# Kernel tuning notes

Measured on AMD Instinct MI355X. Metric: run time of the kernel, lower is better.

Reference implementation:

```python
import jax, jax.numpy as jnp
import numpy as np

SLOPE = 25.0   # fast_sigmoid surrogate slope
THR = 1.0      # snntorch Leaky default threshold


@jax.custom_vjp
def spike(x):
    # Heaviside forward, fast-sigmoid surrogate backward
    return (x > 0).astype(x.dtype)

def _spike_fwd(x):
    return spike(x), x

def _spike_bwd(x, g):
    return (g / (SLOPE * jnp.abs(x) + 1.0) ** 2,)

spike.defvjp(_spike_fwd, _spike_bwd)


def conv2d(x, w, b):
    y = jax.lax.conv_general_dilated(
        x, w, window_strides=(1, 1), padding=((1, 1), (1, 1)),
        dimension_numbers=('NCHW', 'OIHW', 'NCHW'))
    return y + b[None, :, None, None]


def maxpool2(x):
    return jax.lax.reduce_window(x, -jnp.inf, jax.lax.max,
                                 (1, 1, 2, 2), (1, 1, 2, 2), 'VALID')


def bn_inf(x, g, b, m, v):
    # inference-mode BatchNorm2d, eps = 1e-5
    inv = g * jax.lax.rsqrt(v + 1e-5)
    return x * inv[None, :, None, None] + (b - m * inv)[None, :, None, None]


def lif_step(mem, inp, beta):
    # snntorch Leaky, reset_mechanism='subtract', learn_beta (clamped to [0,1])
    b = jnp.clip(beta, 0.0, 1.0)
    reset = jax.lax.stop_gradient((mem > THR).astype(mem.dtype))
    mem_new = b * mem + inp - reset * THR
    spk = spike(mem_new - THR)
    return spk, mem_new


def setup_inputs() -> dict:
    key = jax.random.key(0)
    ks = jax.random.split(key, 20)
    T, B, H, W = 25, 512, 100, 64   # T steps, batch, MAX_LEN, N_MELS
    NUM_CLASSES = 35
    FLAT = 32 * (H // 4) * (W // 4)  # 12800
    f32 = jnp.float32
    inp = {
        'x': jax.random.normal(ks[0], (T, B, H, W), f32),
        'conv1_w': jax.random.normal(ks[1], (16, 1, 3, 3), f32) * 0.2,
        'conv1_b': jnp.zeros((16,), f32),
        'bn1_g': jnp.ones((16,), f32),
        'bn1_b': jnp.zeros((16,), f32),
        'bn1_m': jax.random.normal(ks[2], (16,), f32) * 0.1,
        'bn1_v': jax.random.uniform(ks[3], (16,), f32) + 0.5,
        'conv2_w': jax.random.normal(ks[4], (32, 16, 3, 3), f32) * (1.0 / np.sqrt(16 * 9)),
        'conv2_b': jnp.zeros((32,), f32),
        'bn2_g': jnp.ones((32,), f32),
        'bn2_b': jnp.zeros((32,), f32),
        'bn2_m': jax.random.normal(ks[5], (32,), f32) * 0.1,
        'bn2_v': jax.random.uniform(ks[6], (32,), f32) + 0.5,
        'fc1_w': jax.random.normal(ks[7], (256, FLAT), f32) * (1.0 / np.sqrt(FLAT)),
        'fc1_b': jnp.zeros((256,), f32),
        'fc2_w': jax.random.normal(ks[8], (128, 256), f32) * (1.0 / np.sqrt(256)),
        'fc2_b': jnp.zeros((128,), f32),
        'fc3_w': jax.random.normal(ks[9], (NUM_CLASSES, 128), f32) * (1.0 / np.sqrt(128)),
        'fc3_b': jnp.zeros((NUM_CLASSES,), f32),
        'beta1': jnp.float32(0.9),
        'beta2': jnp.float32(0.9),
        'beta3': jnp.float32(0.9),
    }
    return inp


def reference(x, conv1_w, conv1_b, bn1_g, bn1_b, bn1_m, bn1_v,
              conv2_w, conv2_b, bn2_g, bn2_b, bn2_m, bn2_v,
              fc1_w, fc1_b, fc2_w, fc2_b, fc3_w, fc3_b,
              beta1, beta2, beta3):
    T, B = x.shape[0], x.shape[1]
    # CNN runs once on the time-averaged input
    x_mean = jnp.mean(x, axis=0)[:, None]          # (B, 1, H, W)
    f = maxpool2(jax.nn.relu(bn_inf(conv2d(x_mean, conv1_w, conv1_b), bn1_g, bn1_b, bn1_m, bn1_v)))
    f = maxpool2(jax.nn.relu(bn_inf(conv2d(f, conv2_w, conv2_b), bn2_g, bn2_b, bn2_m, bn2_v)))
    feat = f.reshape(B, -1)                        # (B, FLAT)
    # fc1 input is the same every step (dropout = identity in eval)
    cur1 = feat @ fc1_w.T + fc1_b                  # (B, 256)

    m1 = jnp.zeros((B, fc1_w.shape[0]), x.dtype)
    m2 = jnp.zeros((B, fc2_w.shape[0]), x.dtype)
    m3 = jnp.zeros((B, fc3_w.shape[0]), x.dtype)

    def step(carry, _):
        m1, m2, m3 = carry
        spk1, m1 = lif_step(m1, cur1, beta1)
        spk2, m2 = lif_step(m2, spk1 @ fc2_w.T + fc2_b, beta2)
        spk3, m3 = lif_step(m3, spk2 @ fc3_w.T + fc3_b, beta3)
        return (m1, m2, m3), spk3

    _, out = jax.lax.scan(step, (m1, m2, m3), None, length=T)
    return out                                     # (T, B, NUM_CLASSES)
```

## Files before the change

kernel.cpp:

```cpp
#include <hip/hip_runtime.h>

#define N_P1    (512*16*50*32)
#define N_FEAT  (512*12800)
#define N_PART  (32*512*256)

#define WS_P1    0
#define WS_FEAT  (WS_P1 + N_P1)
#define WS_PART  (WS_FEAT + N_FEAT)
#define WS_S1    0
#define WS_IN2   3276800
#define WS_S2    4915200

__global__ __launch_bounds__(256) void conv1_kernel(const float* __restrict__ x,
                                                    const float* __restrict__ w1,
                                                    const float* __restrict__ cb1,
                                                    const float* __restrict__ g1,
                                                    const float* __restrict__ bb1,
                                                    const float* __restrict__ m1g,
                                                    const float* __restrict__ v1,
                                                    float* __restrict__ p1) {
    __shared__ float xs[22 * 66];
    __shared__ float w1s[144];
    __shared__ float sh1s[16];
    const int b = blockIdx.x, s = blockIdx.y;
    const int tid = threadIdx.x;
    if (tid < 144) {
        int c = tid / 9;
        float inv = g1[c] * rsqrtf(v1[c] + 1e-5f);
        w1s[tid] = w1[tid] * inv;
    }
    if (tid < 16) {
        float inv = g1[tid] * rsqrtf(v1[tid] + 1e-5f);
        sh1s[tid] = cb1[tid] * inv + bb1[tid] - m1g[tid] * inv;
    }
    if (tid < 44) xs[(tid >> 1) * 66 + (tid & 1) * 65] = 0.f;
    const int r0 = s * 20 - 1;
    const size_t TSTR = (size_t)512 * 6400;
    for (int i = tid; i < 22 * 16; i += 256) {
        int lr = i >> 4, cq = i & 15;
        int gr = r0 + lr;
        float4 a0 = make_float4(0.f, 0.f, 0.f, 0.f), a1 = a0, a2 = a0, a3 = a0;
        if (gr >= 0 && gr < 100) {
            const float* px = x + (size_t)b * 6400 + gr * 64 + cq * 4;
            #pragma unroll
            for (int tt = 0; tt < 24; tt += 4) {
                float4 v0 = *(const float4*)(px + (size_t)(tt + 0) * TSTR);
                float4 v1_ = *(const float4*)(px + (size_t)(tt + 1) * TSTR);
                float4 v2_ = *(const float4*)(px + (size_t)(tt + 2) * TSTR);
                float4 v3 = *(const float4*)(px + (size_t)(tt + 3) * TSTR);
                a0.x += v0.x; a0.y += v0.y; a0.z += v0.z; a0.w += v0.w;
                a1.x += v1_.x; a1.y += v1_.y; a1.z += v1_.z; a1.w += v1_.w;
                a2.x += v2_.x; a2.y += v2_.y; a2.z += v2_.z; a2.w += v2_.w;
                a3.x += v3.x; a3.y += v3.y; a3.z += v3.z; a3.w += v3.w;
            }
            float4 v = *(const float4*)(px + (size_t)24 * TSTR);
            a0.x += v.x; a0.y += v.y; a0.z += v.z; a0.w += v.w;
        }
        const float sc = 1.0f / 25.0f;
        float* d = &xs[lr * 66 + 1 + cq * 4];
        d[0] = (a0.x + a1.x + a2.x + a3.x) * sc;
        d[1] = (a0.y + a1.y + a2.y + a3.y) * sc;
        d[2] = (a0.z + a1.z + a2.z + a3.z) * sc;
        d[3] = (a0.w + a1.w + a2.w + a3.w) * sc;
    }
    __syncthreads();
    for (int pos = tid; pos < 320; pos += 256) {
        int phl = pos >> 5, pw = pos & 31;
        int ph = s * 10 + phl;
        float win[4][4];
        #pragma unroll
        for (int a = 0; a < 4; ++a)
            #pragma unroll
            for (int c2 = 0; c2 < 4; ++c2)
                win[a][c2] = xs[(2 * phl + a) * 66 + 2 * pw + c2];
        #pragma unroll 1
        for (int c = 0; c < 16; ++c) {
            float s00 = 0.f, s01 = 0.f, s10 = 0.f, s11 = 0.f;
            #pragma unroll
            for (int dh = 0; dh < 3; ++dh)
                #pragma unroll
                for (int dw = 0; dw < 3; ++dw) {
                    float w = w1s[c * 9 + dh * 3 + dw];
                    s00 = fmaf(win[dh][dw],         w, s00);
                    s01 = fmaf(win[dh][dw + 1],     w, s01);
                    s10 = fmaf(win[dh + 1][dw],     w, s10);
                    s11 = fmaf(win[dh + 1][dw + 1], w, s11);
                }
            float m = fmaxf(fmaxf(s00, s01), fmaxf(s10, s11));
            float val = fmaxf(m + sh1s[c], 0.f);
            p1[(((size_t)b * 16 + c) * 50 + ph) * 32 + pw] = val;
        }
    }
}

__global__ __launch_bounds__(320) void conv2_kernel(const float* __restrict__ p1,
                                                    const float* __restrict__ w2g,
                                                    const float* __restrict__ cb2,
                                                    const float* __restrict__ g2,
                                                    const float* __restrict__ bb2,
                                                    const float* __restrict__ m2g,
                                                    const float* __restrict__ v2,
                                                    float* __restrict__ feat) {
    __shared__ float ins[16 * 12 * 36];
    __shared__ float wl[16 * 9 * 32];
    __shared__ float sh2s[32];
    const int b = blockIdx.x, s = blockIdx.y;
    const int tid = threadIdx.x;
    const int chg = tid & 15, q = (tid >> 4) & 3, phl = tid >> 6;
    const int ph = s * 5 + phl;

    for (int i = tid; i < 192; i += 320) {
        int ci = i / 12, lr = i - ci * 12;
        int gr = s * 10 - 1 + lr;
        float* dst = &ins[(ci * 12 + lr) * 36];
        if (gr >= 0 && gr < 50) {
            const float* src = p1 + (((size_t)b * 16 + ci) * 50 + gr) * 32;
            float4 v0 = *(const float4*)src;
            dst[0] = 0.f; dst[1] = v0.x; dst[2] = v0.y; dst[3] = v0.z;
            #pragma unroll
            for (int qq = 1; qq < 8; ++qq) {
                float4 v = *(const float4*)(src + 4 * qq - 1);
                *(float4*)(dst + 4 * qq) = v;
            }
            dst[32] = src[31];
            dst[33] = 0.f; dst[34] = 0.f; dst[35] = 0.f;
        } else {
            #pragma unroll
            for (int qq = 0; qq < 9; ++qq) *(float4*)(dst + 4 * qq) = make_float4(0.f, 0.f, 0.f, 0.f);
        }
    }
    for (int i = tid; i < 4608; i += 320) {
        int c = i / 144, rem = i - c * 144;
        float inv = g2[c] * rsqrtf(v2[c] + 1e-5f);
        wl[rem * 32 + c] = w2g[i] * inv;
    }
    if (tid < 32) {
        float inv = g2[tid] * rsqrtf(v2[tid] + 1e-5f);
        sh2s[tid] = cb2[tid] * inv + bb2[tid] - m2g[tid] * inv;
    }
    __syncthreads();

    float acc[2][2][8];
    #pragma unroll
    for (int c = 0; c < 2; ++c)
        #pragma unroll
        for (int a = 0; a < 2; ++a)
            #pragma unroll
            for (int xx = 0; xx < 8; ++xx) acc[c][a][xx] = 0.f;
    const int xb = q * 8;
    #pragma unroll 1
    for (int ci = 0; ci < 16; ++ci) {
        float2 wv[9];
        #pragma unroll
        for (int t = 0; t < 9; ++t)
            wv[t] = *(const float2*)&wl[(ci * 9 + t) * 32 + 2 * chg];
        #pragma unroll
        for (int lr4 = 0; lr4 < 4; ++lr4) {
            const float* row = &ins[(ci * 12 + (2 * phl + lr4)) * 36 + xb];
            float v[10];
            float4 t0 = *(const float4*)&row[0];
            float4 t1 = *(const float4*)&row[4];
            float2 t2 = *(const float2*)&row[8];
            v[0]=t0.x; v[1]=t0.y; v[2]=t0.z; v[3]=t0.w;
            v[4]=t1.x; v[5]=t1.y; v[6]=t1.z; v[7]=t1.w;
            v[8]=t2.x; v[9]=t2.y;
            #pragma unroll
            for (int a = 0; a < 2; ++a) {
                const int dh = lr4 - a;
                if (dh >= 0 && dh <= 2) {
                    #pragma unroll
                    for (int dw = 0; dw < 3; ++dw) {
                        float w0 = wv[dh * 3 + dw].x;
                        float w1 = wv[dh * 3 + dw].y;
                        #pragma unroll
                        for (int xx = 0; xx < 8; ++xx) {
                            acc[0][a][xx] = fmaf(v[xx + dw], w0, acc[0][a][xx]);
                            acc[1][a][xx] = fmaf(v[xx + dw], w1, acc[1][a][xx]);
                        }
                    }
                }
            }
        }
    }
    #pragma unroll
    for (int ch = 0; ch < 2; ++ch) {
        const int c = 2 * chg + ch;
        const float sh = sh2s[c];
        #pragma unroll
        for (int p = 0; p < 4; ++p) {
            float m = fmaxf(fmaxf(acc[ch][0][2 * p], acc[ch][0][2 * p + 1]),
                            fmaxf(acc[ch][1][2 * p], acc[ch][1][2 * p + 1]));
            float val = fmaxf(m + sh, 0.f);
            feat[(((size_t)b * 32 + c) * 25 + ph) * 16 + q * 4 + p] = val;
        }
    }
}

__global__ __launch_bounds__(256) void fc1_kernel(const float* __restrict__ feat,
                                                  const float* __restrict__ w,
                                                  float* __restrict__ part) {
    __shared__ float As[16 * 68];
    __shared__ float Bs[16 * 136];
    const int bx = blockIdx.x, by = blockIdx.y, bz = blockIdx.z;
    const int tid = threadIdx.x;
    const int tm = tid >> 4, tn = tid & 15;
    const int r = tid >> 2, cq = tid & 3;
    const int m0 = bx * 64, n0 = by * 128;
    const size_t aBase = (size_t)(m0 + r) * 12800 + bz * 400 + cq * 4;
    const size_t bBase = (size_t)(n0 + r) * 12800 + bz * 400 + cq * 4;
    float acc[4][8];
    #pragma unroll
    for (int i = 0; i < 4; ++i)
        #pragma unroll
        for (int j = 0; j < 8; ++j) acc[i][j] = 0.f;

    for (int kt = 0; kt < 25; ++kt) {
        float4 a0 = *(const float4*)(feat + aBase + kt * 16);
        float4 b0 = *(const float4*)(w    + bBase + kt * 16);
        float4 b1 = *(const float4*)(w    + bBase + (size_t)64 * 12800 + kt * 16);
        __syncthreads();
        As[(cq * 4 + 0) * 68 + r] = a0.x; As[(cq * 4 + 1) * 68 + r] = a0.y;
        As[(cq * 4 + 2) * 68 + r] = a0.z; As[(cq * 4 + 3) * 68 + r] = a0.w;
        Bs[(cq * 4 + 0) * 136 + r]      = b0.x; Bs[(cq * 4 + 1) * 136 + r]      = b0.y;
        Bs[(cq * 4 + 2) * 136 + r]      = b0.z; Bs[(cq * 4 + 3) * 136 + r]      = b0.w;
        Bs[(cq * 4 + 0) * 136 + 64 + r] = b1.x; Bs[(cq * 4 + 1) * 136 + 64 + r] = b1.y;
        Bs[(cq * 4 + 2) * 136 + 64 + r] = b1.z; Bs[(cq * 4 + 3) * 136 + 64 + r] = b1.w;
        __syncthreads();
        #pragma unroll
        for (int kk = 0; kk < 16; ++kk) {
            float4 av  = *(const float4*)&As[kk * 68 + tm * 4];
            float4 bv0 = *(const float4*)&Bs[kk * 136 + tn * 8];
            float4 bv1 = *(const float4*)&Bs[kk * 136 + tn * 8 + 4];
            float a_[4] = {av.x, av.y, av.z, av.w};
            float b_[8] = {bv0.x, bv0.y, bv0.z, bv0.w, bv1.x, bv1.y, bv1.z, bv1.w};
            #pragma unroll
            for (int i = 0; i < 4; ++i)
                #pragma unroll
                for (int j = 0; j < 8; ++j)
                    acc[i][j] = fmaf(a_[i], b_[j], acc[i][j]);
        }
    }
    #pragma unroll
    for (int i = 0; i < 4; ++i) {
        float* dst = &part[(size_t)bz * 131072 + (size_t)(m0 + tm * 4 + i) * 256 + n0 + tn * 8];
        *(float4*)dst       = make_float4(acc[i][0], acc[i][1], acc[i][2], acc[i][3]);
        *(float4*)(dst + 4) = make_float4(acc[i][4], acc[i][5], acc[i][6], acc[i][7]);
    }
}

__global__ __launch_bounds__(256) void lif1_kernel(const float* __restrict__ part,
                                                   const float* __restrict__ b1g,
                                                   const float* __restrict__ pb1,
                                                   float* __restrict__ S1) {
    const int i = blockIdx.x * 256 + threadIdx.x;
    const int k = i & 255;
    float cu = b1g[k];
    #pragma unroll 8
    for (int z = 0; z < 32; ++z) cu += part[(size_t)z * 131072 + i];
    const float be = fminf(fmaxf(pb1[0], 0.f), 1.f);
    float m = 0.f;
    #pragma unroll
    for (int t = 0; t < 25; ++t) {
        float r = (m > 1.f) ? 1.f : 0.f;
        m = fmaf(be, m, cu) - r;
        S1[(size_t)t * 131072 + i] = (m > 1.f) ? 1.f : 0.f;
    }
}

__global__ __launch_bounds__(256) void fc2g_kernel(const float* __restrict__ S1,
                                                   const float* __restrict__ w2g,
                                                   const float* __restrict__ b2g,
                                                   float* __restrict__ in2) {
    __shared__ float As[16 * 36];
    __shared__ float Bs[16 * 136];
    const int m0 = blockIdx.x * 32;
    const int tid = threadIdx.x;
    const int tm = tid >> 4, tn = tid & 15;
    float acc[2][8];
    #pragma unroll
    for (int i = 0; i < 2; ++i)
        #pragma unroll
        for (int j = 0; j < 8; ++j) acc[i][j] = 0.f;

    for (int kt = 0; kt < 16; ++kt) {
        float4 av = make_float4(0.f, 0.f, 0.f, 0.f);
        if (tid < 128) {
            int r = tid >> 2, cq = tid & 3;
            av = *(const float4*)&S1[(size_t)(m0 + r) * 256 + kt * 16 + cq * 4];
        }
        int rb = tid >> 1, kb = (tid & 1) * 8;
        float4 bv0 = *(const float4*)&w2g[rb * 256 + kt * 16 + kb];
        float4 bv1 = *(const float4*)&w2g[rb * 256 + kt * 16 + kb + 4];
        __syncthreads();
        if (tid < 128) {
            int r = tid >> 2, cq = tid & 3;
            As[(cq * 4 + 0) * 36 + r] = av.x; As[(cq * 4 + 1) * 36 + r] = av.y;
            As[(cq * 4 + 2) * 36 + r] = av.z; As[(cq * 4 + 3) * 36 + r] = av.w;
        }
        Bs[(kb + 0) * 136 + rb] = bv0.x; Bs[(kb + 1) * 136 + rb] = bv0.y;
        Bs[(kb + 2) * 136 + rb] = bv0.z; Bs[(kb + 3) * 136 + rb] = bv0.w;
        Bs[(kb + 4) * 136 + rb] = bv1.x; Bs[(kb + 5) * 136 + rb] = bv1.y;
        Bs[(kb + 6) * 136 + rb] = bv1.z; Bs[(kb + 7) * 136 + rb] = bv1.w;
        __syncthreads();
        #pragma unroll
        for (int kk = 0; kk < 16; ++kk) {
            float2 a2 = *(const float2*)&As[kk * 36 + tm * 2];
            float4 bv0_ = *(const float4*)&Bs[kk * 136 + tn * 8];
            float4 bv1_ = *(const float4*)&Bs[kk * 136 + tn * 8 + 4];
            float b_[8] = {bv0_.x, bv0_.y, bv0_.z, bv0_.w, bv1_.x, bv1_.y, bv1_.z, bv1_.w};
            #pragma unroll
            for (int j = 0; j < 8; ++j) {
                acc[0][j] = fmaf(a2.x, b_[j], acc[0][j]);
                acc[1][j] = fmaf(a2.y, b_[j], acc[1][j]);
            }
        }
    }
    float4 bb0 = *(const float4*)&b2g[tn * 8];
    float4 bb1 = *(const float4*)&b2g[tn * 8 + 4];
    #pragma unroll
    for (int i = 0; i < 2; ++i) {
        float* dst = &in2[(size_t)(m0 + tm * 2 + i) * 128 + tn * 8];
        *(float4*)dst       = make_float4(acc[i][0] + bb0.x, acc[i][1] + bb0.y,
                                          acc[i][2] + bb0.z, acc[i][3] + bb0.w);
        *(float4*)(dst + 4) = make_float4(acc[i][4] + bb1.x, acc[i][5] + bb1.y,
                                          acc[i][6] + bb1.z, acc[i][7] + bb1.w);
    }
}

__global__ __launch_bounds__(256) void lif2_kernel(const float* __restrict__ in2,
                                                   const float* __restrict__ pb2,
                                                   float* __restrict__ S2) {
    const int i = blockIdx.x * 256 + threadIdx.x;
    const float be = fminf(fmaxf(pb2[0], 0.f), 1.f);
    float m = 0.f;
    #pragma unroll
    for (int t = 0; t < 25; ++t) {
        float r = (m > 1.f) ? 1.f : 0.f;
        m = fmaf(be, m, in2[(size_t)t * 65536 + i]) - r;
        S2[(size_t)t * 65536 + i] = (m > 1.f) ? 1.f : 0.f;
    }
}

__global__ __launch_bounds__(64) void fc3l_kernel(const float* __restrict__ S2,
                                                  const float* __restrict__ w3g,
                                                  const float* __restrict__ b3g,
                                                  const float* __restrict__ pb3,
                                                  float* __restrict__ out) {
    __shared__ float w3T[128 * 36];
    __shared__ float s2row[128];
    const int b = blockIdx.x;
    const int lane = threadIdx.x;
    for (int i = lane; i < 4480; i += 64) {
        int j = i >> 7, k = i & 127;
        w3T[k * 36 + j] = w3g[i];
    }
    const float be = fminf(fmaxf(pb3[0], 0.f), 1.f);
    const float bias = (lane < 35) ? b3g[lane] : 0.f;
    float m = 0.f;
    __syncthreads();
    for (int t = 0; t < 25; ++t) {
        float2 v = *(const float2*)&S2[(size_t)t * 65536 + b * 128 + lane * 2];
        *(float2*)&s2row[lane * 2] = v;
        __syncthreads();
        if (lane < 35) {
            float a = bias;
            #pragma unroll 8
            for (int k = 0; k < 128; ++k)
                a = fmaf(s2row[k], w3T[k * 36 + lane], a);
            float r = (m > 1.f) ? 1.f : 0.f;
            m = fmaf(be, m, a) - r;
            out[((size_t)t * 512 + b) * 35 + lane] = (m > 1.f) ? 1.f : 0.f;
        }
        __syncthreads();
    }
}

extern "C" void kernel_launch(void* const* d_in, const int* in_sizes, int n_in,
                              void* d_out, int out_size, void* d_ws, size_t ws_size,
                              hipStream_t stream) {
    const float* x     = (const float*)d_in[0];
    const float* c1w   = (const float*)d_in[1];
    const float* c1b   = (const float*)d_in[2];
    const float* bn1g  = (const float*)d_in[3];
    const float* bn1b  = (const float*)d_in[4];
    const float* bn1m  = (const float*)d_in[5];
    const float* bn1v  = (const float*)d_in[6];
    const float* c2w   = (const float*)d_in[7];
    const float* c2b   = (const float*)d_in[8];
    const float* bn2g  = (const float*)d_in[9];
    const float* bn2b  = (const float*)d_in[10];
    const float* bn2m  = (const float*)d_in[11];
    const float* bn2v  = (const float*)d_in[12];
    const float* fc1w  = (const float*)d_in[13];
    const float* fc1b  = (const float*)d_in[14];
    const float* fc2w  = (const float*)d_in[15];
    const float* fc2b  = (const float*)d_in[16];
    const float* fc3w  = (const float*)d_in[17];
    const float* fc3b  = (const float*)d_in[18];
    const float* beta1 = (const float*)d_in[19];
    const float* beta2 = (const float*)d_in[20];
    const float* beta3 = (const float*)d_in[21];
    float* ws  = (float*)d_ws;
    float* out = (float*)d_out;

    conv1_kernel<<<dim3(512, 5), 256, 0, stream>>>(x, c1w, c1b, bn1g, bn1b, bn1m, bn1v,
                                                   ws + WS_P1);
    conv2_kernel<<<dim3(512, 5), 320, 0, stream>>>(ws + WS_P1, c2w, c2b, bn2g, bn2b, bn2m, bn2v,
                                                   ws + WS_FEAT);
    fc1_kernel<<<dim3(8, 2, 32), 256, 0, stream>>>(ws + WS_FEAT, fc1w, ws + WS_PART);
    lif1_kernel<<<512, 256, 0, stream>>>(ws + WS_PART, fc1b, beta1, ws + WS_S1);
    fc2g_kernel<<<400, 256, 0, stream>>>(ws + WS_S1, fc2w, fc2b, ws + WS_IN2);
    lif2_kernel<<<256, 256, 0, stream>>>(ws + WS_IN2, beta2, ws + WS_S2);
    fc3l_kernel<<<512, 64, 0, stream>>>(ws + WS_S2, fc3w, fc3b, beta3, out);
}
```

Before: 328.0 us.

## Enlarge fc1 tiles, prefetch GEMM loads, split fc3 into GEMM plus LIF kernels

conv1 now runs with 384 threads so each thread handles one input load slot and one output position instead of looping. fc1 moves to a 128x128 tile with an 8x8 per-thread micro-tile and register prefetch of the next K slice. fc2 gets the same register-prefetch double buffering. The serial per-batch fc3+LIF kernel is replaced by a batched GEMM over all 25 time steps followed by an elementwise LIF scan. This aims to raise arithmetic intensity and parallelism, at the cost of higher register pressure in fc1 and an extra workspace round trip for fc3.

```diff
diff --git a/kernel.cpp b/kernel.cpp
--- a/kernel.cpp
+++ b/kernel.cpp
@@ -10,8 +10,9 @@
 #define WS_S1    0
 #define WS_IN2   3276800
 #define WS_S2    4915200
-
-__global__ __launch_bounds__(256) void conv1_kernel(const float* __restrict__ x,
+#define WS_IN3   6553600
+
+__global__ __launch_bounds__(384) void conv1_kernel(const float* __restrict__ x,
                                                     const float* __restrict__ w1,
                                                     const float* __restrict__ cb1,
                                                     const float* __restrict__ g1,
@@ -29,15 +30,19 @@
         float inv = g1[c] * rsqrtf(v1[c] + 1e-5f);
         w1s[tid] = w1[tid] * inv;
     }
-    if (tid < 16) {
-        float inv = g1[tid] * rsqrtf(v1[tid] + 1e-5f);
-        sh1s[tid] = cb1[tid] * inv + bb1[tid] - m1g[tid] * inv;
-    }
-    if (tid < 44) xs[(tid >> 1) * 66 + (tid & 1) * 65] = 0.f;
+    if (tid >= 144 && tid < 160) {
+        int c = tid - 144;
+        float inv = g1[c] * rsqrtf(v1[c] + 1e-5f);
+        sh1s[c] = cb1[c] * inv + bb1[c] - m1g[c] * inv;
+    }
+    if (tid >= 160 && tid < 204) {
+        int q = tid - 160;
+        xs[(q >> 1) * 66 + (q & 1) * 65] = 0.f;
+    }
     const int r0 = s * 20 - 1;
     const size_t TSTR = (size_t)512 * 6400;
-    for (int i = tid; i < 22 * 16; i += 256) {
-        int lr = i >> 4, cq = i & 15;
+    if (tid < 352) {
+        int lr = tid >> 4, cq = tid & 15;
         int gr = r0 + lr;
         float4 a0 = make_float4(0.f, 0.f, 0.f, 0.f), a1 = a0, a2 = a0, a3 = a0;
         if (gr >= 0 && gr < 100) {
@@ -64,8 +69,8 @@
         d[3] = (a0.w + a1.w + a2.w + a3.w) * sc;
     }
     __syncthreads();
-    for (int pos = tid; pos < 320; pos += 256) {
-        int phl = pos >> 5, pw = pos & 31;
+    if (tid < 320) {
+        int phl = tid >> 5, pw = tid & 31;
         int ph = s * 10 + phl;
         float win[4][4];
         #pragma unroll
@@ -199,50 +204,57 @@
 __global__ __launch_bounds__(256) void fc1_kernel(const float* __restrict__ feat,
                                                   const float* __restrict__ w,
                                                   float* __restrict__ part) {
-    __shared__ float As[16 * 68];
+    __shared__ float As[16 * 136];
     __shared__ float Bs[16 * 136];
     const int bx = blockIdx.x, by = blockIdx.y, bz = blockIdx.z;
     const int tid = threadIdx.x;
     const int tm = tid >> 4, tn = tid & 15;
     const int r = tid >> 2, cq = tid & 3;
-    const int m0 = bx * 64, n0 = by * 128;
+    const int m0 = bx * 128, n0 = by * 128;
     const size_t aBase = (size_t)(m0 + r) * 12800 + bz * 400 + cq * 4;
     const size_t bBase = (size_t)(n0 + r) * 12800 + bz * 400 + cq * 4;
-    float acc[4][8];
-    #pragma unroll
-    for (int i = 0; i < 4; ++i)
-        #pragma unroll
-        for (int j = 0; j < 8; ++j) acc[i][j] = 0.f;
+    float acc[8][8] = {};
+    float4 a0 = *(const float4*)(feat + aBase);
+    float4 a1 = *(const float4*)(feat + aBase + (size_t)64 * 12800);
+    float4 b0 = *(const float4*)(w    + bBase);
+    float4 b1 = *(const float4*)(w    + bBase + (size_t)64 * 12800);
 
     for (int kt = 0; kt < 25; ++kt) {
-        float4 a0 = *(const float4*)(feat + aBase + kt * 16);
-        float4 b0 = *(const float4*)(w    + bBase + kt * 16);
-        float4 b1 = *(const float4*)(w    + bBase + (size_t)64 * 12800 + kt * 16);
-        __syncthreads();
-        As[(cq * 4 + 0) * 68 + r] = a0.x; As[(cq * 4 + 1) * 68 + r] = a0.y;
-        As[(cq * 4 + 2) * 68 + r] = a0.z; As[(cq * 4 + 3) * 68 + r] = a0.w;
+        __syncthreads();
+        As[(cq * 4 + 0) * 136 + r]      = a0.x; As[(cq * 4 + 1) * 136 + r]      = a0.y;
+        As[(cq * 4 + 2) * 136 + r]      = a0.z; As[(cq * 4 + 3) * 136 + r]      = a0.w;
+        As[(cq * 4 + 0) * 136 + 64 + r] = a1.x; As[(cq * 4 + 1) * 136 + 64 + r] = a1.y;
+        As[(cq * 4 + 2) * 136 + 64 + r] = a1.z; As[(cq * 4 + 3) * 136 + 64 + r] = a1.w;
         Bs[(cq * 4 + 0) * 136 + r]      = b0.x; Bs[(cq * 4 + 1) * 136 + r]      = b0.y;
         Bs[(cq * 4 + 2) * 136 + r]      = b0.z; Bs[(cq * 4 + 3) * 136 + r]      = b0.w;
         Bs[(cq * 4 + 0) * 136 + 64 + r] = b1.x; Bs[(cq * 4 + 1) * 136 + 64 + r] = b1.y;
         Bs[(cq * 4 + 2) * 136 + 64 + r] = b1.z; Bs[(cq * 4 + 3) * 136 + 64 + r] = b1.w;
         __syncthreads();
+        if (kt < 24) {
+            const int o = (kt + 1) * 16;
+            a0 = *(const float4*)(feat + aBase + o);
+            a1 = *(const float4*)(feat + aBase + (size_t)64 * 12800 + o);
+            b0 = *(const float4*)(w    + bBase + o);
+            b1 = *(const float4*)(w    + bBase + (size_t)64 * 12800 + o);
+        }
         #pragma unroll
         for (int kk = 0; kk < 16; ++kk) {
-            float4 av  = *(const float4*)&As[kk * 68 + tm * 4];
+            float4 av0 = *(const float4*)&As[kk * 136 + tm * 8];
+            float4 av1 = *(const float4*)&As[kk * 136 + tm * 8 + 4];
             float4 bv0 = *(const float4*)&Bs[kk * 136 + tn * 8];
             float4 bv1 = *(const float4*)&Bs[kk * 136 + tn * 8 + 4];
-            float a_[4] = {av.x, av.y, av.z, av.w};
+            float a_[8] = {av0.x, av0.y, av0.z, av0.w, av1.x, av1.y, av1.z, av1.w};
             float b_[8] = {bv0.x, bv0.y, bv0.z, bv0.w, bv1.x, bv1.y, bv1.z, bv1.w};
             #pragma unroll
-            for (int i = 0; i < 4; ++i)
+            for (int i = 0; i < 8; ++i)
                 #pragma unroll
                 for (int j = 0; j < 8; ++j)
                     acc[i][j] = fmaf(a_[i], b_[j], acc[i][j]);
         }
     }
     #pragma unroll
-    for (int i = 0; i < 4; ++i) {
-        float* dst = &part[(size_t)bz * 131072 + (size_t)(m0 + tm * 4 + i) * 256 + n0 + tn * 8];
+    for (int i = 0; i < 8; ++i) {
+        float* dst = &part[(size_t)bz * 131072 + (size_t)(m0 + tm * 8 + i) * 256 + n0 + tn * 8];
         *(float4*)dst       = make_float4(acc[i][0], acc[i][1], acc[i][2], acc[i][3]);
         *(float4*)(dst + 4) = make_float4(acc[i][4], acc[i][5], acc[i][6], acc[i][7]);
     }
@@ -276,38 +288,37 @@
     const int m0 = blockIdx.x * 32;
     const int tid = threadIdx.x;
     const int tm = tid >> 4, tn = tid & 15;
-    float acc[2][8];
-    #pragma unroll
-    for (int i = 0; i < 2; ++i)
-        #pragma unroll
-        for (int j = 0; j < 8; ++j) acc[i][j] = 0.f;
+    const int ra = tid >> 2, cqa = tid & 3;
+    const int rb = tid >> 1, kb = (tid & 1) * 8;
+    float acc[2][8] = {};
+    float4 av = make_float4(0.f, 0.f, 0.f, 0.f);
+    if (tid < 128) av = *(const float4*)&S1[(size_t)(m0 + ra) * 256 + cqa * 4];
+    float4 bv0 = *(const float4*)&w2g[rb * 256 + kb];
+    float4 bv1 = *(const float4*)&w2g[rb * 256 + kb + 4];
 
     for (int kt = 0; kt < 16; ++kt) {
-        float4 av = make_float4(0.f, 0.f, 0.f, 0.f);
+        __syncthreads();
         if (tid < 128) {
-            int r = tid >> 2, cq = tid & 3;
-            av = *(const float4*)&S1[(size_t)(m0 + r) * 256 + kt * 16 + cq * 4];
-        }
-        int rb = tid >> 1, kb = (tid & 1) * 8;
-        float4 bv0 = *(const float4*)&w2g[rb * 256 + kt * 16 + kb];
-        float4 bv1 = *(const float4*)&w2g[rb * 256 + kt * 16 + kb + 4];
-        __syncthreads();
-        if (tid < 128) {
-            int r = tid >> 2, cq = tid & 3;
-            As[(cq * 4 + 0) * 36 + r] = av.x; As[(cq * 4 + 1) * 36 + r] = av.y;
-            As[(cq * 4 + 2) * 36 + r] = av.z; As[(cq * 4 + 3) * 36 + r] = av.w;
+            As[(cqa * 4 + 0) * 36 + ra] = av.x; As[(cqa * 4 + 1) * 36 + ra] = av.y;
+            As[(cqa * 4 + 2) * 36 + ra] = av.z; As[(cqa * 4 + 3) * 36 + ra] = av.w;
         }
         Bs[(kb + 0) * 136 + rb] = bv0.x; Bs[(kb + 1) * 136 + rb] = bv0.y;
         Bs[(kb + 2) * 136 + rb] = bv0.z; Bs[(kb + 3) * 136 + rb] = bv0.w;
         Bs[(kb + 4) * 136 + rb] = bv1.x; Bs[(kb + 5) * 136 + rb] = bv1.y;
         Bs[(kb + 6) * 136 + rb] = bv1.z; Bs[(kb + 7) * 136 + rb] = bv1.w;
         __syncthreads();
+        if (kt < 15) {
+            const int o = (kt + 1) * 16;
+            if (tid < 128) av = *(const float4*)&S1[(size_t)(m0 + ra) * 256 + o + cqa * 4];
+            bv0 = *(const float4*)&w2g[rb * 256 + o + kb];
+            bv1 = *(const float4*)&w2g[rb * 256 + o + kb + 4];
+        }
         #pragma unroll
         for (int kk = 0; kk < 16; ++kk) {
             float2 a2 = *(const float2*)&As[kk * 36 + tm * 2];
-            float4 bv0_ = *(const float4*)&Bs[kk * 136 + tn * 8];
-            float4 bv1_ = *(const float4*)&Bs[kk * 136 + tn * 8 + 4];
-            float b_[8] = {bv0_.x, bv0_.y, bv0_.z, bv0_.w, bv1_.x, bv1_.y, bv1_.z, bv1_.w};
+            float4 bw0 = *(const float4*)&Bs[kk * 136 + tn * 8];
+            float4 bw1 = *(const float4*)&Bs[kk * 136 + tn * 8 + 4];
+            float b_[8] = {bw0.x, bw0.y, bw0.z, bw0.w, bw1.x, bw1.y, bw1.z, bw1.w};
             #pragma unroll
             for (int j = 0; j < 8; ++j) {
                 acc[0][j] = fmaf(a2.x, b_[j], acc[0][j]);
@@ -341,37 +352,64 @@
     }
 }
 
-__global__ __launch_bounds__(64) void fc3l_kernel(const float* __restrict__ S2,
-                                                  const float* __restrict__ w3g,
-                                                  const float* __restrict__ b3g,
-                                                  const float* __restrict__ pb3,
-                                                  float* __restrict__ out) {
-    __shared__ float w3T[128 * 36];
-    __shared__ float s2row[128];
-    const int b = blockIdx.x;
-    const int lane = threadIdx.x;
-    for (int i = lane; i < 4480; i += 64) {
-        int j = i >> 7, k = i & 127;
-        w3T[k * 36 + j] = w3g[i];
-    }
+__global__ __launch_bounds__(256) void fc3g_kernel(const float* __restrict__ S2,
+                                                   const float* __restrict__ w3g,
+                                                   const float* __restrict__ b3g,
+                                                   float* __restrict__ in3) {
+    __shared__ float As[16 * 36];
+    __shared__ float Bs[16 * 48];
+    const int m0 = blockIdx.x * 32;
+    const int tid = threadIdx.x;
+    const int tm = tid >> 4, tn = tid & 15;
+    float acc[2][3] = {};
+    for (int kt = 0; kt < 8; ++kt) {
+        __syncthreads();
+        if (tid < 128) {
+            int r = tid >> 2, cq = tid & 3;
+            float4 av = *(const float4*)&S2[(size_t)(m0 + r) * 128 + kt * 16 + cq * 4];
+            As[(cq * 4 + 0) * 36 + r] = av.x; As[(cq * 4 + 1) * 36 + r] = av.y;
+            As[(cq * 4 + 2) * 36 + r] = av.z; As[(cq * 4 + 3) * 36 + r] = av.w;
+        }
+        for (int i = tid; i < 560; i += 256) {
+            int kk = i / 35, c = i - kk * 35;
+            Bs[kk * 48 + c] = w3g[c * 128 + kt * 16 + kk];
+        }
+        __syncthreads();
+        #pragma unroll
+        for (int kk = 0; kk < 16; ++kk) {
+            float2 a2 = *(const float2*)&As[kk * 36 + tm * 2];
+            float w0 = Bs[kk * 48 + tn];
+            float w1 = Bs[kk * 48 + tn + 16];
+            float w2 = Bs[kk * 48 + tn + 32];
+            acc[0][0] = fmaf(a2.x, w0, acc[0][0]); acc[1][0] = fmaf(a2.y, w0, acc[1][0]);
+            acc[0][1] = fmaf(a2.x, w1, acc[0][1]); acc[1][1] = fmaf(a2.y, w1, acc[1][1]);
+            acc[0][2] = fmaf(a2.x, w2, acc[0][2]); acc[1][2] = fmaf(a2.y, w2, acc[1][2]);
+        }
+    }
+    const float bias0 = b3g[tn];
+    const float bias1 = b3g[tn + 16];
+    const float bias2 = (tn < 3) ? b3g[tn + 32] : 0.f;
+    #pragma unroll
+    for (int i = 0; i < 2; ++i) {
+        const size_t row = (size_t)(m0 + tm * 2 + i) * 35;
+        in3[row + tn]      = acc[i][0] + bias0;
+        in3[row + tn + 16] = acc[i][1] + bias1;
+        if (tn < 3) in3[row + tn + 32] = acc[i][2] + bias2;
+    }
+}
+
+__global__ __launch_bounds__(256) void lif3_kernel(const float* __restrict__ in3,
+                                                   const float* __restrict__ pb3,
+                                                   float* __restrict__ out) {
+    const int i = blockIdx.x * 256 + threadIdx.x;
+    if (i >= 17920) return;
     const float be = fminf(fmaxf(pb3[0], 0.f), 1.f);
-    const float bias = (lane < 35) ? b3g[lane] : 0.f;
     float m = 0.f;
-    __syncthreads();
+    #pragma unroll
     for (int t = 0; t < 25; ++t) {
-        float2 v = *(const float2*)&S2[(size_t)t * 65536 + b * 128 + lane * 2];
-        *(float2*)&s2row[lane * 2] = v;
-        __syncthreads();
-        if (lane < 35) {
-            float a = bias;
-            #pragma unroll 8
-            for (int k = 0; k < 128; ++k)
-                a = fmaf(s2row[k], w3T[k * 36 + lane], a);
-            float r = (m > 1.f) ? 1.f : 0.f;
-            m = fmaf(be, m, a) - r;
-            out[((size_t)t * 512 + b) * 35 + lane] = (m > 1.f) ? 1.f : 0.f;
-        }
-        __syncthreads();
+        float r = (m > 1.f) ? 1.f : 0.f;
+        m = fmaf(be, m, in3[(size_t)t * 17920 + i]) - r;
+        out[(size_t)t * 17920 + i] = (m > 1.f) ? 1.f : 0.f;
     }
 }
 
@@ -403,13 +441,14 @@
     float* ws  = (float*)d_ws;
     float* out = (float*)d_out;
 
-    conv1_kernel<<<dim3(512, 5), 256, 0, stream>>>(x, c1w, c1b, bn1g, bn1b, bn1m, bn1v,
+    conv1_kernel<<<dim3(512, 5), 384, 0, stream>>>(x, c1w, c1b, bn1g, bn1b, bn1m, bn1v,
                                                    ws + WS_P1);
     conv2_kernel<<<dim3(512, 5), 320, 0, stream>>>(ws + WS_P1, c2w, c2b, bn2g, bn2b, bn2m, bn2v,
                                                    ws + WS_FEAT);
-    fc1_kernel<<<dim3(8, 2, 32), 256, 0, stream>>>(ws + WS_FEAT, fc1w, ws + WS_PART);
+    fc1_kernel<<<dim3(4, 2, 32), 256, 0, stream>>>(ws + WS_FEAT, fc1w, ws + WS_PART);
     lif1_kernel<<<512, 256, 0, stream>>>(ws + WS_PART, fc1b, beta1, ws + WS_S1);
     fc2g_kernel<<<400, 256, 0, stream>>>(ws + WS_S1, fc2w, fc2b, ws + WS_IN2);
     lif2_kernel<<<256, 256, 0, stream>>>(ws + WS_IN2, beta2, ws + WS_S2);
-    fc3l_kernel<<<512, 64, 0, stream>>>(ws + WS_S2, fc3w, fc3b, beta3, out);
-}
+    fc3g_kernel<<<400, 256, 0, stream>>>(ws + WS_S2, fc3w, fc3b, ws + WS_IN3);
+    lif3_kernel<<<70, 256, 0, stream>>>(ws + WS_IN3, beta3, out);
+}
```

New measurement: 300.4 us. 8.4% less time.
